# Optimization experiments

Hardware: AMD Instinct MI355X
Metric: run time of the kernel (lower is better)

The kernel has to match this reference:

```python
import jax, jax.numpy as jnp
import numpy as np

B, H = 65536, 512


def setup_inputs() -> dict:
    key = jax.random.key(0)
    ks = jax.random.split(key, 10)
    s = 1.0 / np.sqrt(H)  # torch nn.Linear default init range
    uni = lambda k, shape: jax.random.uniform(k, shape, jnp.float32, -s, s)
    return {
        "inputs": jax.random.normal(ks[0], (B, H), jnp.float32),
        "short_term_memory": jax.random.normal(ks[1], (B, H), jnp.float32),
        "Wf": uni(ks[2], (H, H)), "bf": uni(ks[3], (H,)),
        "Wi": uni(ks[4], (H, H)), "bi": uni(ks[5], (H,)),
        "Wg": uni(ks[6], (H, H)), "bg": uni(ks[7], (H,)),
        "Wo": uni(ks[8], (H, H)), "bo": uni(ks[9], (H,)),
    }


def reference(inputs, short_term_memory, Wf, bf, Wi, bi, Wg, bg, Wo, bo):
    z = inputs + short_term_memory  # [B, H]
    # ForgetGate: OVERWRITES long-term memory (previous cell state never read).
    c = jax.nn.sigmoid(z @ Wf.T + bf)
    # InputGate: c += sigmoid(...) * tanh(...)
    c = c + jax.nn.sigmoid(z @ Wi.T + bi) * jnp.tanh(z @ Wg.T + bg)
    # OutputGate: h = tanh(c) * sigmoid(...)
    h = jnp.tanh(c) * jax.nn.sigmoid(z @ Wo.T + bo)
    return jnp.stack((c, h))  # [2, B, H]: new long-term and short-term memory
```

## Files before the change

### kernel.cpp

```cpp
#include <hip/hip_runtime.h>

typedef __bf16 bf16x8 __attribute__((ext_vector_type(8)));
typedef float  f32x4  __attribute__((ext_vector_type(4)));

#define LOG2E 1.4426950408889634f

static __device__ __forceinline__ float fexp2(float x) { return __builtin_amdgcn_exp2f(x); }
static __device__ __forceinline__ float frcp(float x)  { return __builtin_amdgcn_rcpf(x); }
static __device__ __forceinline__ float fsigmoid(float x) { return frcp(1.0f + fexp2(-LOG2E * x)); }
static __device__ __forceinline__ float ftanh(float x)    { return 2.0f * frcp(1.0f + fexp2(-2.0f * LOG2E * x)) - 1.0f; }

__global__ __launch_bounds__(256) void wpack(const float* __restrict__ Wf,
                                             const float* __restrict__ Wi,
                                             const float* __restrict__ Wg,
                                             const float* __restrict__ Wo,
                                             __bf16* __restrict__ Wp)
{
    int idx = blockIdx.x * 256 + threadIdx.x;
    int kg  = idx & 63;
    int j   = (idx >> 6) & 511;
    int g   = idx >> 15;
    const float* src = (g == 0) ? Wf : (g == 1) ? Wi : (g == 2) ? Wg : Wo;
    const float4* s4 = (const float4*)(src + j * 512 + kg * 8);
    float4 v0 = s4[0], v1 = s4[1];
    bf16x8 o;
    o[0] = (__bf16)v0.x; o[1] = (__bf16)v0.y; o[2] = (__bf16)v0.z; o[3] = (__bf16)v0.w;
    o[4] = (__bf16)v1.x; o[5] = (__bf16)v1.y; o[6] = (__bf16)v1.z; o[7] = (__bf16)v1.w;
    int cn = j >> 4;
    int ks = kg >> 2;
    int lt = (j & 15) + (kg & 3) * 16;
    size_t dst = ((size_t)(((g * 32 + cn) * 16 + ks) * 64 + lt)) * 8;
    *(bf16x8*)(Wp + dst) = o;
}

__global__ __launch_bounds__(512, 2) void lstm_main(
    const float* __restrict__ xin, const float* __restrict__ stm,
    const __bf16* __restrict__ Wp,
    const float* __restrict__ bfv, const float* __restrict__ biv,
    const float* __restrict__ bgv, const float* __restrict__ bov,
    float* __restrict__ out)
{
    __shared__ unsigned char zs[131072];
    const int tid  = threadIdx.x;
    const int lane = tid & 63;
    const int wv   = tid >> 6;
    const int l15  = lane & 15;
    const int lq   = lane >> 4;
    const int row0 = blockIdx.x * 128;

    {
        const float* xb = xin + (size_t)row0 * 512;
        const float* sb = stm + (size_t)row0 * 512;
        #pragma unroll
        for (int it = 0; it < 16; ++it) {
            int idx = it * 512 + tid;
            int row = idx >> 6;
            int kg  = idx & 63;
            const float4* x4 = (const float4*)(xb + row * 512 + kg * 8);
            const float4* s4 = (const float4*)(sb + row * 512 + kg * 8);
            float4 a0 = x4[0], a1 = x4[1];
            float4 b0 = s4[0], b1 = s4[1];
            bf16x8 p;
            p[0] = (__bf16)(a0.x + b0.x); p[1] = (__bf16)(a0.y + b0.y);
            p[2] = (__bf16)(a0.z + b0.z); p[3] = (__bf16)(a0.w + b0.w);
            p[4] = (__bf16)(a1.x + b1.x); p[5] = (__bf16)(a1.y + b1.y);
            p[6] = (__bf16)(a1.z + b1.z); p[7] = (__bf16)(a1.w + b1.w);
            int rb   = row >> 5;
            int kk   = kg >> 1;
            int slot = ((row & 31) + (kg & 1) * 32) ^ (kk & 7);
            *(bf16x8*)(zs + rb * 32768 + kk * 1024 + slot * 16) = p;
        }
    }
    __syncthreads();

    const int kkoff = lq >> 1;
    const int s0    = l15 + (lq & 1) * 32;
    const int koffb = kkoff << 10;

    for (int ci = 0; ci < 4; ++ci) {
        const int cn   = ci * 8 + wv;
        const int colj = cn * 16 + l15;

        const __bf16* bp0 = Wp + ((size_t)((  0 + cn) * 16)) * 512 + lane * 8;
        const __bf16* bp1 = Wp + ((size_t)(( 32 + cn) * 16)) * 512 + lane * 8;
        const __bf16* bp2 = Wp + ((size_t)(( 64 + cn) * 16)) * 512 + lane * 8;
        const __bf16* bp3 = Wp + ((size_t)(( 96 + cn) * 16)) * 512 + lane * 8;

        float bias0 = bfv[colj], bias1 = biv[colj], bias2 = bgv[colj], bias3 = bov[colj];
        f32x4 acc[8][4];
        #pragma unroll
        for (int m = 0; m < 8; ++m) {
            #pragma unroll
            for (int r = 0; r < 4; ++r) {
                acc[m][0][r] = bias0; acc[m][1][r] = bias1;
                acc[m][2][r] = bias2; acc[m][3][r] = bias3;
            }
        }

        #pragma unroll 2
        for (int ks = 0; ks < 16; ++ks) {
            const int kk7 = ((2 * ks) & 7) | kkoff;
            const int t0  = ((s0 ^ kk7) << 4) + ks * 2048 + koffb;
            bf16x8 b0 = *(const bf16x8*)(bp0 + ks * 512);
            bf16x8 b1 = *(const bf16x8*)(bp1 + ks * 512);
            bf16x8 b2 = *(const bf16x8*)(bp2 + ks * 512);
            bf16x8 b3 = *(const bf16x8*)(bp3 + ks * 512);
            bf16x8 a[8];
            #pragma unroll
            for (int m = 0; m < 8; ++m)
                a[m] = *(const bf16x8*)(zs + (m >> 1) * 32768 + (m & 1) * 256 + t0);
            #pragma unroll
            for (int m = 0; m < 8; ++m) {
                acc[m][0] = __builtin_amdgcn_mfma_f32_16x16x32_bf16(a[m], b0, acc[m][0], 0, 0, 0);
                acc[m][1] = __builtin_amdgcn_mfma_f32_16x16x32_bf16(a[m], b1, acc[m][1], 0, 0, 0);
                acc[m][2] = __builtin_amdgcn_mfma_f32_16x16x32_bf16(a[m], b2, acc[m][2], 0, 0, 0);
                acc[m][3] = __builtin_amdgcn_mfma_f32_16x16x32_bf16(a[m], b3, acc[m][3], 0, 0, 0);
            }
        }

        #pragma unroll
        for (int m = 0; m < 8; ++m) {
            #pragma unroll
            for (int r = 0; r < 4; ++r) {
                float F = acc[m][0][r], I = acc[m][1][r];
                float G = acc[m][2][r], O = acc[m][3][r];
                float c = fsigmoid(F) + fsigmoid(I) * ftanh(G);
                float h = ftanh(c) * fsigmoid(O);
                int row = row0 + m * 16 + lq * 4 + r;
                int o   = row * 512 + colj;
                out[o] = c;
                out[33554432 + o] = h;
            }
        }
    }
}

extern "C" void kernel_launch(void* const* d_in, const int* in_sizes, int n_in,
                              void* d_out, int out_size, void* d_ws, size_t ws_size,
                              hipStream_t stream) {
    const float* xin = (const float*)d_in[0];
    const float* stm = (const float*)d_in[1];
    const float* Wf  = (const float*)d_in[2];
    const float* bf_ = (const float*)d_in[3];
    const float* Wi  = (const float*)d_in[4];
    const float* bi_ = (const float*)d_in[5];
    const float* Wg  = (const float*)d_in[6];
    const float* bg_ = (const float*)d_in[7];
    const float* Wo  = (const float*)d_in[8];
    const float* bo_ = (const float*)d_in[9];
    __bf16* Wp = (__bf16*)d_ws;

    wpack<<<512, 256, 0, stream>>>(Wf, Wi, Wg, Wo, Wp);
    lstm_main<<<512, 512, 0, stream>>>(xin, stm, Wp, bf_, bi_, bg_, bo_, (float*)d_out);
}
```

Measured before the change: 192.9 us.

## Warp-specialize LSTM kernel into MFMA producer and activation/store consumer waves

Splits each block into four producer waves that run the bf16 MFMA GEMM and four consumer waves that apply the gate nonlinearities and write outputs. The two sides hand off accumulators through an LDS ring buffer guarded by spin flags. Block row tile shrinks from 128 to 64 with twice as many blocks, and packed weights are re-laid out so the four gates for a column tile are contiguous. B-tile loads use inline-asm double buffering with explicit vmcnt waits. The aim is to overlap epilogue transcendentals and global stores with matrix math, at the cost of halving per-wave MFMA reuse, and of spin-wait and LDS-ordering risks.

```diff
diff --git a/kernel.cpp b/kernel.cpp
--- a/kernel.cpp
+++ b/kernel.cpp
@@ -29,7 +29,7 @@
     int cn = j >> 4;
     int ks = kg >> 2;
     int lt = (j & 15) + (kg & 3) * 16;
-    size_t dst = ((size_t)(((g * 32 + cn) * 16 + ks) * 64 + lt)) * 8;
+    size_t dst = ((size_t)(((cn * 16 + ks) * 4 + g) * 64 + lt)) * 8;
     *(bf16x8*)(Wp + dst) = o;
 }
 
@@ -40,19 +40,25 @@
     const float* __restrict__ bgv, const float* __restrict__ bov,
     float* __restrict__ out)
 {
-    __shared__ unsigned char zs[131072];
+    __shared__ unsigned char zs[65536];
+    __shared__ unsigned char ring[4][5][4096];
+    __shared__ int pflag[4];
+    __shared__ int cflag[4];
     const int tid  = threadIdx.x;
     const int lane = tid & 63;
     const int wv   = tid >> 6;
+    const int pid  = wv & 3;
     const int l15  = lane & 15;
     const int lq   = lane >> 4;
-    const int row0 = blockIdx.x * 128;
+    const int row0 = blockIdx.x * 64;
+
+    if (tid < 4) { pflag[tid] = 0; cflag[tid] = 0; }
 
     {
         const float* xb = xin + (size_t)row0 * 512;
         const float* sb = stm + (size_t)row0 * 512;
         #pragma unroll
-        for (int it = 0; it < 16; ++it) {
+        for (int it = 0; it < 8; ++it) {
             int idx = it * 512 + tid;
             int row = idx >> 6;
             int kg  = idx & 63;
@@ -73,64 +79,133 @@
     }
     __syncthreads();
 
-    const int kkoff = lq >> 1;
-    const int s0    = l15 + (lq & 1) * 32;
-    const int koffb = kkoff << 10;
-
-    for (int ci = 0; ci < 4; ++ci) {
-        const int cn   = ci * 8 + wv;
-        const int colj = cn * 16 + l15;
-
-        const __bf16* bp0 = Wp + ((size_t)((  0 + cn) * 16)) * 512 + lane * 8;
-        const __bf16* bp1 = Wp + ((size_t)(( 32 + cn) * 16)) * 512 + lane * 8;
-        const __bf16* bp2 = Wp + ((size_t)(( 64 + cn) * 16)) * 512 + lane * 8;
-        const __bf16* bp3 = Wp + ((size_t)(( 96 + cn) * 16)) * 512 + lane * 8;
-
-        float bias0 = bfv[colj], bias1 = biv[colj], bias2 = bgv[colj], bias3 = bov[colj];
-        f32x4 acc[8][4];
-        #pragma unroll
-        for (int m = 0; m < 8; ++m) {
+    volatile int* pf = (volatile int*)&pflag[pid];
+    volatile int* cf = (volatile int*)&cflag[pid];
+
+    if (wv < 4) {
+        const int kkoff = lq >> 1;
+        const int sl0   = l15 + (lq & 1) * 32;
+        const int koffb = kkoff << 10;
+
+#define LOADB_ASM(B0, B1, B2, B3, KS) { \
+    const char* a_ = bp + (KS) * 4096; \
+    asm volatile("global_load_dwordx4 %0, %4, off\n\t" \
+                 "global_load_dwordx4 %1, %4, off offset:1024\n\t" \
+                 "global_load_dwordx4 %2, %4, off offset:2048\n\t" \
+                 "global_load_dwordx4 %3, %4, off offset:3072" \
+                 : "=&v"(B0), "=&v"(B1), "=&v"(B2), "=&v"(B3) : "v"(a_) : "memory"); }
+#define WAITV4 { asm volatile("s_waitcnt vmcnt(4)" ::: "memory"); __builtin_amdgcn_sched_barrier(0); }
+#define WAITV0 { asm volatile("s_waitcnt vmcnt(0)" ::: "memory"); __builtin_amdgcn_sched_barrier(0); }
+#define DOMFMA(B0, B1, B2, B3, KS) { \
+    const int kk7_ = ((2 * (KS)) & 7) | kkoff; \
+    const int t0_  = ((sl0 ^ kk7_) << 4) + (KS) * 2048 + koffb; \
+    bf16x8 a0_ = *(const bf16x8*)(zs + t0_); \
+    bf16x8 a1_ = *(const bf16x8*)(zs + t0_ + 256); \
+    bf16x8 a2_ = *(const bf16x8*)(zs + 32768 + t0_); \
+    bf16x8 a3_ = *(const bf16x8*)(zs + 32768 + t0_ + 256); \
+    __builtin_amdgcn_s_setprio(1); \
+    acc[0][0] = __builtin_amdgcn_mfma_f32_16x16x32_bf16(a0_, B0, acc[0][0], 0, 0, 0); \
+    acc[1][0] = __builtin_amdgcn_mfma_f32_16x16x32_bf16(a1_, B0, acc[1][0], 0, 0, 0); \
+    acc[2][0] = __builtin_amdgcn_mfma_f32_16x16x32_bf16(a2_, B0, acc[2][0], 0, 0, 0); \
+    acc[3][0] = __builtin_amdgcn_mfma_f32_16x16x32_bf16(a3_, B0, acc[3][0], 0, 0, 0); \
+    acc[0][1] = __builtin_amdgcn_mfma_f32_16x16x32_bf16(a0_, B1, acc[0][1], 0, 0, 0); \
+    acc[1][1] = __builtin_amdgcn_mfma_f32_16x16x32_bf16(a1_, B1, acc[1][1], 0, 0, 0); \
+    acc[2][1] = __builtin_amdgcn_mfma_f32_16x16x32_bf16(a2_, B1, acc[2][1], 0, 0, 0); \
+    acc[3][1] = __builtin_amdgcn_mfma_f32_16x16x32_bf16(a3_, B1, acc[3][1], 0, 0, 0); \
+    acc[0][2] = __builtin_amdgcn_mfma_f32_16x16x32_bf16(a0_, B2, acc[0][2], 0, 0, 0); \
+    acc[1][2] = __builtin_amdgcn_mfma_f32_16x16x32_bf16(a1_, B2, acc[1][2], 0, 0, 0); \
+    acc[2][2] = __builtin_amdgcn_mfma_f32_16x16x32_bf16(a2_, B2, acc[2][2], 0, 0, 0); \
+    acc[3][2] = __builtin_amdgcn_mfma_f32_16x16x32_bf16(a3_, B2, acc[3][2], 0, 0, 0); \
+    acc[0][3] = __builtin_amdgcn_mfma_f32_16x16x32_bf16(a0_, B3, acc[0][3], 0, 0, 0); \
+    acc[1][3] = __builtin_amdgcn_mfma_f32_16x16x32_bf16(a1_, B3, acc[1][3], 0, 0, 0); \
+    acc[2][3] = __builtin_amdgcn_mfma_f32_16x16x32_bf16(a2_, B3, acc[2][3], 0, 0, 0); \
+    acc[3][3] = __builtin_amdgcn_mfma_f32_16x16x32_bf16(a3_, B3, acc[3][3], 0, 0, 0); \
+    __builtin_amdgcn_s_setprio(0); }
+
+        int slot = 0;
+        for (int pass = 0; pass < 8; ++pass) {
+            const int cn   = pass * 4 + pid;
+            const int colj = cn * 16 + l15;
+            const char* bp = (const char*)Wp + (size_t)cn * 65536 + (size_t)lane * 16;
+
+            float bias0 = bfv[colj], bias1 = biv[colj];
+            float bias2 = bgv[colj], bias3 = bov[colj];
+            f32x4 acc[4][4];
+            #pragma unroll
+            for (int m = 0; m < 4; ++m) {
+                #pragma unroll
+                for (int r = 0; r < 4; ++r) {
+                    acc[m][0][r] = bias0; acc[m][1][r] = bias1;
+                    acc[m][2][r] = bias2; acc[m][3][r] = bias3;
+                }
+            }
+
+            bf16x8 p0, p1, p2, p3, q0, q1, q2, q3;
+            asm volatile("s_waitcnt vmcnt(0)" ::: "memory");
+            __builtin_amdgcn_sched_barrier(0);
+            LOADB_ASM(p0, p1, p2, p3, 0)
+            #pragma unroll
+            for (int ks = 0; ks < 16; ks += 2) {
+                LOADB_ASM(q0, q1, q2, q3, ks + 1)
+                WAITV4
+                DOMFMA(p0, p1, p2, p3, ks)
+                if (ks + 2 < 16) {
+                    LOADB_ASM(p0, p1, p2, p3, ks + 2)
+                    WAITV4
+                } else {
+                    WAITV0
+                }
+                DOMFMA(q0, q1, q2, q3, ks + 1)
+            }
+
+            #pragma unroll
+            for (int m = 0; m < 4; ++m) {
+                int q = pass * 4 + m;
+                if (q >= 5) {
+                    while (*cf < q - 4) __builtin_amdgcn_s_sleep(2);
+                    asm volatile("" ::: "memory");
+                }
+                unsigned char* sb = &ring[pid][slot][0] + lane * 16;
+                *(f32x4*)(sb)        = acc[m][0];
+                *(f32x4*)(sb + 1024) = acc[m][1];
+                *(f32x4*)(sb + 2048) = acc[m][2];
+                *(f32x4*)(sb + 3072) = acc[m][3];
+                if (++slot == 5) slot = 0;
+            }
+            asm volatile("s_waitcnt lgkmcnt(0)" ::: "memory");
+            if (lane == 0) *pf = pass * 4 + 4;
+        }
+#undef LOADB_ASM
+#undef WAITV4
+#undef WAITV0
+#undef DOMFMA
+    } else {
+        int slot = 0;
+        for (int q = 0; q < 32; ++q) {
+            while (*pf < q + 1) __builtin_amdgcn_s_sleep(2);
+            asm volatile("" ::: "memory");
+            __builtin_amdgcn_sched_barrier(0);
+            const unsigned char* sb = &ring[pid][slot][0] + lane * 16;
+            f32x4 vF = *(const f32x4*)(sb);
+            f32x4 vI = *(const f32x4*)(sb + 1024);
+            f32x4 vG = *(const f32x4*)(sb + 2048);
+            f32x4 vO = *(const f32x4*)(sb + 3072);
+
+            const int pass = q >> 2, m = q & 3;
+            const int cn   = pass * 4 + pid;
+            const int colj = cn * 16 + l15;
             #pragma unroll
             for (int r = 0; r < 4; ++r) {
-                acc[m][0][r] = bias0; acc[m][1][r] = bias1;
-                acc[m][2][r] = bias2; acc[m][3][r] = bias3;
-            }
-        }
-
-        #pragma unroll 2
-        for (int ks = 0; ks < 16; ++ks) {
-            const int kk7 = ((2 * ks) & 7) | kkoff;
-            const int t0  = ((s0 ^ kk7) << 4) + ks * 2048 + koffb;
-            bf16x8 b0 = *(const bf16x8*)(bp0 + ks * 512);
-            bf16x8 b1 = *(const bf16x8*)(bp1 + ks * 512);
-            bf16x8 b2 = *(const bf16x8*)(bp2 + ks * 512);
-            bf16x8 b3 = *(const bf16x8*)(bp3 + ks * 512);
-            bf16x8 a[8];
-            #pragma unroll
-            for (int m = 0; m < 8; ++m)
-                a[m] = *(const bf16x8*)(zs + (m >> 1) * 32768 + (m & 1) * 256 + t0);
-            #pragma unroll
-            for (int m = 0; m < 8; ++m) {
-                acc[m][0] = __builtin_amdgcn_mfma_f32_16x16x32_bf16(a[m], b0, acc[m][0], 0, 0, 0);
-                acc[m][1] = __builtin_amdgcn_mfma_f32_16x16x32_bf16(a[m], b1, acc[m][1], 0, 0, 0);
-                acc[m][2] = __builtin_amdgcn_mfma_f32_16x16x32_bf16(a[m], b2, acc[m][2], 0, 0, 0);
-                acc[m][3] = __builtin_amdgcn_mfma_f32_16x16x32_bf16(a[m], b3, acc[m][3], 0, 0, 0);
-            }
-        }
-
-        #pragma unroll
-        for (int m = 0; m < 8; ++m) {
-            #pragma unroll
-            for (int r = 0; r < 4; ++r) {
-                float F = acc[m][0][r], I = acc[m][1][r];
-                float G = acc[m][2][r], O = acc[m][3][r];
-                float c = fsigmoid(F) + fsigmoid(I) * ftanh(G);
-                float h = ftanh(c) * fsigmoid(O);
+                float c = fsigmoid(vF[r]) + fsigmoid(vI[r]) * ftanh(vG[r]);
+                float h = ftanh(c) * fsigmoid(vO[r]);
                 int row = row0 + m * 16 + lq * 4 + r;
                 int o   = row * 512 + colj;
                 out[o] = c;
                 out[33554432 + o] = h;
             }
+            asm volatile("s_waitcnt lgkmcnt(0)" ::: "memory");
+            if (lane == 0) *cf = q + 1;
+            if (++slot == 5) slot = 0;
         }
     }
 }
@@ -151,5 +226,5 @@
     __bf16* Wp = (__bf16*)d_ws;
 
     wpack<<<512, 256, 0, stream>>>(Wf, Wi, Wg, Wo, Wp);
-    lstm_main<<<512, 512, 0, stream>>>(xin, stm, Wp, bf_, bi_, bg_, bo_, (float*)d_out);
+    lstm_main<<<1024, 512, 0, stream>>>(xin, stm, Wp, bf_, bi_, bg_, bo_, (float*)d_out);
 }
```

New measurement: 226.3 us. 1.17x slower.
